# Performance work log

Measured on AMD Instinct MI355X. Metric: run time of the kernel, lower is better.

Reference implementation:

```python
import jax, jax.numpy as jnp
import numpy as np

NUM_GRAPHS = 512
EPS = 1e-5

def squash(x):
    # capsule squash: (|x|^2 / (1 + |x|^2)) * x / |x|
    n2 = jnp.sum(x * x, axis=-1, keepdims=True)
    return (n2 / (1.0 + n2)) * x * jax.lax.rsqrt(n2 + 1e-12)

def setup_inputs():
    key = jax.random.key(0)
    ks = jax.random.split(key, 16)
    N, E, F, H, L, C = 100000, 600000, 128, 128, 3, 2
    x = jax.random.normal(ks[0], (N, F), jnp.float32)
    edge_index = jax.random.randint(ks[1], (2, E), 0, N)
    batch = jnp.sort(jax.random.randint(ks[2], (N,), 0, NUM_GRAPHS))
    def lin(k, i, o):
        return (jax.random.normal(k, (i, o), jnp.float32) / np.sqrt(i)).astype(jnp.float32)
    return {
        'x': x, 'edge_index': edge_index, 'batch': batch,
        'bn_gamma': jnp.ones((F,), jnp.float32), 'bn_beta': jnp.zeros((F,), jnp.float32),
        'W0': lin(ks[3], F, H), 'b0': jnp.zeros((H,), jnp.float32),
        'W1': lin(ks[4], H, H), 'b1': jnp.zeros((H,), jnp.float32),
        'W2': lin(ks[5], H, H), 'b2': jnp.zeros((H,), jnp.float32),
        'tar_w': (jax.random.normal(ks[6], (L, H), jnp.float32) / np.sqrt(H)).astype(jnp.float32),
        'lin1_w': lin(ks[7], 3 * H, H), 'lin1_b': jnp.zeros((H,), jnp.float32),
        'lin2_w': lin(ks[8], H, C), 'lin2_b': jnp.zeros((C,), jnp.float32),
    }

def reference(x, edge_index, batch, bn_gamma, bn_beta, W0, b0, W1, b1, W2, b2,
              tar_w, lin1_w, lin1_b, lin2_w, lin2_b):
    N, G = x.shape[0], NUM_GRAPHS
    # input BatchNorm1d (training-mode batch statistics)
    mu = jnp.mean(x, 0)
    var = jnp.var(x, 0)
    h = (x - mu) * jax.lax.rsqrt(var + EPS) * bn_gamma + bn_beta
    # remove_self_loops + add_remaining_self_loops ~= append diagonal with weight 1
    loops = jnp.arange(N)
    src = jnp.concatenate([edge_index[0], loops])
    dst = jnp.concatenate([edge_index[1], loops])
    w = jnp.ones((src.shape[0],), h.dtype)
    # GCN symmetric normalization D^-1/2 A D^-1/2
    deg = jax.ops.segment_sum(w, dst, num_segments=N)
    dinv = jax.lax.rsqrt(jnp.maximum(deg, 1e-12))
    norm = dinv[src] * w * dinv[dst]  # [E+N]
    ones_n = jnp.ones((N,), h.dtype)
    cnt = jax.ops.segment_sum(ones_n, batch, num_segments=G)  # nodes per graph
    cnt_safe = jnp.maximum(cnt, 1.0)[:, None]
    graph_rep = jnp.zeros((G, 3 * W0.shape[1]), h.dtype)
    loss_stability = jnp.zeros((), h.dtype)
    for i, (W, b) in enumerate([(W0, b0), (W1, b1), (W2, b2)]):
        m = h @ W  # [N, H]
        agg = jax.ops.segment_sum(norm[:, None] * m[src], dst, num_segments=N) + b
        h = squash(agg)
        loss_stability = loss_stability + jnp.mean((agg - h) ** 2)
        # Task-Aware Readout: node attention then fused sum / mean / max scatters
        attn = h @ tar_w[i]  # [N]
        x_wsum = jax.ops.segment_sum(attn[:, None] * h, batch, num_segments=G)
        x_mean = jax.ops.segment_sum(h, batch, num_segments=G) / cnt_safe
        x_max = jax.ops.segment_max(h, batch, num_segments=G)
        x_max = jnp.where(cnt[:, None] > 0, x_max, 0.0)
        graph_rep = graph_rep + jnp.concatenate([x_wsum, x_mean, x_max], axis=-1)
    z = jax.nn.relu(graph_rep @ lin1_w + lin1_b)
    z = z @ lin2_w + lin2_b
    return jax.nn.log_softmax(z, axis=-1)
```

## Files before the change

kernel.cpp:

```cpp
#include <hip/hip_runtime.h>
#include <hip/hip_bf16.h>
#include <math.h>

#define BN_EPS 1e-5f
#define BN_BLOCKS 512
#define NCHUNK 256

typedef __attribute__((ext_vector_type(8)))  short short8v;
typedef __attribute__((ext_vector_type(16))) float f32x16;

__device__ __forceinline__ unsigned short f2bf(float f){
  union { float f; unsigned u; } v; v.f = f;
  unsigned r = v.u + 0x7FFFu + ((v.u >> 16) & 1u);
  return (unsigned short)(r >> 16);
}
__device__ __forceinline__ float bf2f(unsigned short b){
  union { unsigned u; float f; } v; v.u = ((unsigned)b) << 16;
  return v.f;
}
__device__ __forceinline__ float2 bfpair(unsigned u){
  union { unsigned u; float f; } lo, hi;
  lo.u = u << 16;
  hi.u = u & 0xFFFF0000u;
  return make_float2(lo.f, hi.f);
}
__device__ __forceinline__ unsigned packbf(float a, float b){
  return (unsigned)f2bf(a) | ((unsigned)f2bf(b) << 16);
}

__global__ __launch_bounds__(256) void bn_part(const float* __restrict__ x,
                                               float* __restrict__ part, int total4){
  const float4* x4 = (const float4*)x;
  int stride = gridDim.x * blockDim.x;
  float4 s = make_float4(0.f,0.f,0.f,0.f);
  float4 q = make_float4(0.f,0.f,0.f,0.f);
  for (int idx = blockIdx.x*blockDim.x + threadIdx.x; idx < total4; idx += stride){
    float4 v = x4[idx];
    s.x += v.x; s.y += v.y; s.z += v.z; s.w += v.w;
    q.x += v.x*v.x; q.y += v.y*v.y; q.z += v.z*v.z; q.w += v.w*v.w;
  }
  __shared__ float4 shs[256], shq[256];
  shs[threadIdx.x] = s; shq[threadIdx.x] = q;
  __syncthreads();
  if (threadIdx.x < 32){
    int c4 = threadIdx.x;
    float4 ts = shs[c4], tq = shq[c4];
    #pragma unroll
    for (int j = 1; j < 8; ++j){
      float4 os = shs[c4 + j*32], oq = shq[c4 + j*32];
      ts.x += os.x; ts.y += os.y; ts.z += os.z; ts.w += os.w;
      tq.x += oq.x; tq.y += oq.y; tq.z += oq.z; tq.w += oq.w;
    }
    float* pb = part + (size_t)blockIdx.x * 256;
    *(float4*)(pb + c4*4)       = ts;
    *(float4*)(pb + 128 + c4*4) = tq;
  }
}

__global__ __launch_bounds__(256) void bn_reduce(const float* __restrict__ part,
                                                 const float* __restrict__ gamma,
                                                 const float* __restrict__ beta,
                                                 float* __restrict__ scale,
                                                 float* __restrict__ shift, int N){
  int t = threadIdx.x;
  float a0=0.f,a1=0.f,a2=0.f,a3=0.f,a4=0.f,a5=0.f,a6=0.f,a7=0.f;
  for (int b = 0; b < BN_BLOCKS; b += 8){
    a0 += part[(size_t)(b+0)*256 + t];
    a1 += part[(size_t)(b+1)*256 + t];
    a2 += part[(size_t)(b+2)*256 + t];
    a3 += part[(size_t)(b+3)*256 + t];
    a4 += part[(size_t)(b+4)*256 + t];
    a5 += part[(size_t)(b+5)*256 + t];
    a6 += part[(size_t)(b+6)*256 + t];
    a7 += part[(size_t)(b+7)*256 + t];
  }
  float acc = ((a0+a1)+(a2+a3)) + ((a4+a5)+(a6+a7));
  __shared__ float sh[256];
  sh[t] = acc;
  __syncthreads();
  if (t < 128){
    float mu  = sh[t] / (float)N;
    float var = sh[t+128] / (float)N - mu*mu;
    float sc  = gamma[t] * rsqrtf(var + BN_EPS);
    scale[t] = sc;
    shift[t] = beta[t] - mu*sc;
  }
}


__global__ __launch_bounds__(256) void chunk_hist(const int* __restrict__ dst,
                                                  int* __restrict__ hist2,
                                                  int E, int NB, int CH){
  __shared__ int lh[512];
  for (int i = threadIdx.x; i < NB; i += 256) lh[i] = 0;
  __syncthreads();
  int c = blockIdx.x;
  int e0 = c*CH, e1 = min(e0 + CH, E);
  for (int e = e0 + threadIdx.x; e < e1; e += 256)
    atomicAdd(&lh[dst[e] >> 8], 1);
  __syncthreads();
  for (int i = threadIdx.x; i < NB; i += 256)
    hist2[c*NB + i] = lh[i];
}

__global__ __launch_bounds__(512) void chunk_scan(const int* __restrict__ hist2,
                                                  int* __restrict__ offs2,
                                                  int* __restrict__ bbase,
                                                  int NB, int E){
  __shared__ int tot[512];
  int b = threadIdx.x;
  int total = 0;
  if (b < NB){
    for (int c = 0; c < NCHUNK; c += 8){
      int h0 = hist2[(c+0)*NB + b], h1 = hist2[(c+1)*NB + b];
      int h2 = hist2[(c+2)*NB + b], h3 = hist2[(c+3)*NB + b];
      int h4 = hist2[(c+4)*NB + b], h5 = hist2[(c+5)*NB + b];
      int h6 = hist2[(c+6)*NB + b], h7 = hist2[(c+7)*NB + b];
      total += ((h0+h1)+(h2+h3)) + ((h4+h5)+(h6+h7));
    }
  }
  tot[b] = (b < NB) ? total : 0;
  __syncthreads();
  int v = tot[b];
  for (int d = 1; d < 512; d <<= 1){
    int u = (b >= d) ? tot[b-d] : 0;
    __syncthreads();
    tot[b] += u;
    __syncthreads();
  }
  if (b < NB){
    int base = tot[b] - v;
    bbase[b] = base;
    int run = base;
    for (int c = 0; c < NCHUNK; c += 8){
      int h0 = hist2[(c+0)*NB + b], h1 = hist2[(c+1)*NB + b];
      int h2 = hist2[(c+2)*NB + b], h3 = hist2[(c+3)*NB + b];
      int h4 = hist2[(c+4)*NB + b], h5 = hist2[(c+5)*NB + b];
      int h6 = hist2[(c+6)*NB + b], h7 = hist2[(c+7)*NB + b];
      offs2[(c+0)*NB + b] = run; run += h0;
      offs2[(c+1)*NB + b] = run; run += h1;
      offs2[(c+2)*NB + b] = run; run += h2;
      offs2[(c+3)*NB + b] = run; run += h3;
      offs2[(c+4)*NB + b] = run; run += h4;
      offs2[(c+5)*NB + b] = run; run += h5;
      offs2[(c+6)*NB + b] = run; run += h6;
      offs2[(c+7)*NB + b] = run; run += h7;
    }
  }
  if (b == 0) bbase[NB] = E;
}

__global__ __launch_bounds__(256) void chunk_scatter(const int* __restrict__ src,
                                                     const int* __restrict__ dst,
                                                     const int* __restrict__ offs2,
                                                     unsigned* __restrict__ ebuf,
                                                     int E, int NB, int CH){
  __shared__ int lcur[512];
  int c = blockIdx.x;
  for (int i = threadIdx.x; i < NB; i += 256) lcur[i] = offs2[c*NB + i];
  __syncthreads();
  int e0 = c*CH, e1 = min(e0 + CH, E);
  for (int e = e0 + threadIdx.x; e < e1; e += 256){
    int d = dst[e];
    int b = d >> 8;
    int pos = atomicAdd(&lcur[b], 1);
    ebuf[pos] = ((unsigned)(d & 255) << 24) | (unsigned)src[e];
  }
}

__global__ __launch_bounds__(256) void bucket_sort(const unsigned* __restrict__ ebuf,
                                                   const int* __restrict__ bbase,
                                                   int* __restrict__ csrs,
                                                   int* __restrict__ rowstart,
                                                   float* __restrict__ dinv,
                                                   int N, int E, int NB){
  int b = blockIdx.x;
  int base = bbase[b];
  int end  = bbase[b+1];
  int len  = end - base;
  int tid = threadIdx.x;
  __shared__ int cnt[256];
  __shared__ int pref[256];
  cnt[tid] = 0;
  __syncthreads();
  for (int i = tid; i < len; i += 256)
    atomicAdd(&cnt[ebuf[base + i] >> 24], 1);
  __syncthreads();
  int v = cnt[tid];
  pref[tid] = v;
  __syncthreads();
  for (int d = 1; d < 256; d <<= 1){
    int u = (tid >= d) ? pref[tid-d] : 0;
    __syncthreads();
    pref[tid] += u;
    __syncthreads();
  }
  int excl = pref[tid] - v;
  int node = b*256 + tid;
  if (node < N){
    rowstart[node] = base + excl;
    dinv[node] = rsqrtf((float)v + 1.0f);
  }
  cnt[tid] = excl;
  __syncthreads();
  for (int i = tid; i < len; i += 256){
    unsigned r = ebuf[base + i];
    int pos = atomicAdd(&cnt[r >> 24], 1);
    csrs[base + pos] = (int)(r & 0xFFFFFFu);
  }
  if (b == NB-1 && tid == 0) rowstart[N] = E;
}

__global__ void gbounds(const int* __restrict__ batch, int* __restrict__ gstart, int N, int G){
  int g = blockIdx.x*blockDim.x + threadIdx.x;
  if (g > G) return;
  int lo = 0, hi = N;
  while (lo < hi){ int mid = (lo+hi)>>1; if (batch[mid] < g) lo = mid+1; else hi = mid; }
  gstart[g] = lo;
}

__global__ void prep_w(const float* __restrict__ W0, const float* __restrict__ W1,
                       const float* __restrict__ W2, const float* __restrict__ scale,
                       unsigned short* __restrict__ Wh){
  int idx = blockIdx.x*blockDim.x + threadIdx.x;
  if (idx >= 3*16384) return;
  int l = idx >> 14, r = idx & 16383, c = r >> 7, k = r & 127;
  const float* W = (l==0) ? W0 : (l==1) ? W1 : W2;
  float v = W[k*128 + c];
  if (l == 0) v *= scale[k];
  Wh[idx] = f2bf(v);
}

__global__ __launch_bounds__(128) void prep_bias0(const float* __restrict__ b0,
                                                  const float* __restrict__ shift,
                                                  const float* __restrict__ W0,
                                                  float* __restrict__ bias0p){
  int j = threadIdx.x;
  __shared__ float sh[128];
  sh[j] = shift[j];
  __syncthreads();
  float s = b0[j];
  for (int c = 0; c < 128; ++c) s += sh[c] * W0[c*128 + j];
  bias0p[j] = s;
}

template<int CVT>
__global__ __launch_bounds__(512) void gemm_mfma(
    const float* __restrict__ A32, const unsigned short* __restrict__ A16,
    const unsigned short* __restrict__ Bh, unsigned short* __restrict__ C, int N){
  __shared__ unsigned short Ah[64*128];
  int tid = threadIdx.x;
  int r0 = blockIdx.x * 64;
  int w = tid >> 6, lane = tid & 63;
  int rt = w & 1;
  int ct = (w >> 1) * 32;
  int lrow = 32*rt + (lane & 31);
  int khalf = lane >> 5;
  int c0 = ct + (lane & 31);
  const unsigned short* bh0 = Bh + (size_t)c0*128 + khalf*8;

  short8v bhf[8];
  #pragma unroll
  for (int s = 0; s < 8; ++s) bhf[s] = *(const short8v*)(bh0 + s*16);

  if (CVT){
    #pragma unroll
    for (int it = 0; it < 4; ++it){
      int idx = tid + it*512;
      int row = idx >> 5;
      int c4  = idx & 31;
      int r = r0 + row;
      float4 av = (r < N) ? *(const float4*)(A32 + (size_t)r*128 + c4*4)
                          : make_float4(0.f,0.f,0.f,0.f);
      int byte0 = (c4*8) ^ ((row & 15) << 4);
      uint2 p = make_uint2(packbf(av.x, av.y), packbf(av.z, av.w));
      *(uint2*)((char*)Ah + row*256 + byte0) = p;
    }
  } else {
    #pragma unroll
    for (int it = 0; it < 2; ++it){
      int idx = tid + it*512;
      int row = idx >> 4;
      int c8  = idx & 15;
      int r = r0 + row;
      uint4 v = (r < N) ? *(const uint4*)(A16 + (size_t)r*128 + c8*8)
                        : make_uint4(0,0,0,0);
      int byte0 = (c8*16) ^ ((row & 15) << 4);
      *(uint4*)((char*)Ah + row*256 + byte0) = v;
    }
  }
  __syncthreads();

  f32x16 acc = {};
  const char* AhB = (const char*)Ah + lrow*256;
  int sw = (lrow & 15) << 4;
  #pragma unroll
  for (int s = 0; s < 8; ++s){
    int abyte = (s*32 + khalf*16) ^ sw;
    short8v a = *(const short8v*)(AhB + abyte);
    acc = __builtin_amdgcn_mfma_f32_32x32x16_bf16(a, bhf[s], acc, 0, 0, 0);
  }

  #pragma unroll
  for (int r = 0; r < 16; ++r){
    int row = r0 + 32*rt + (r & 3) + 8*(r >> 2) + 4*khalf;
    if (row < N) C[(size_t)row*128 + c0] = f2bf(acc[r]);
  }
}

__global__ __launch_bounds__(256) void gather_squash(
    const unsigned short* __restrict__ m, const int* __restrict__ rowstart,
    const int* __restrict__ csrs, const float* __restrict__ dinv,
    const float* __restrict__ bias, const float* __restrict__ tar,
    unsigned short* __restrict__ h, float* __restrict__ attn, int N){
  int node = blockIdx.x*8 + (threadIdx.x >> 5);
  if (node >= N) return;
  int lane = threadIdx.x & 31;
  const uint2* m2 = (const uint2*)m;
  float dv = dinv[node];
  float sn = dv*dv;
  uint2 sv = m2[(size_t)node*32 + lane];
  float2 p0 = bfpair(sv.x), p1 = bfpair(sv.y);
  float a0 = p0.x*sn, a1 = p0.y*sn, a2 = p1.x*sn, a3 = p1.y*sn;
  int j0 = rowstart[node], j1 = rowstart[node+1];

  for (int base = j0; base < j1; base += 32){
    int cnt = j1 - base; if (cnt > 32) cnt = 32;
    int sidx = 0; float swt = 0.f;
    if (lane < cnt){
      sidx = csrs[base + lane];
      swt  = dinv[sidx] * dv;
    }
    int t = 0;
    for (; t + 4 <= cnt; t += 4){
      int s0 = __shfl(sidx, t, 32),   s1 = __shfl(sidx, t+1, 32);
      int s2 = __shfl(sidx, t+2, 32), s3 = __shfl(sidx, t+3, 32);
      float w0 = __shfl(swt, t, 32),   w1 = __shfl(swt, t+1, 32);
      float w2 = __shfl(swt, t+2, 32), w3 = __shfl(swt, t+3, 32);
      uint2 u0 = m2[(size_t)s0*32 + lane];
      uint2 u1 = m2[(size_t)s1*32 + lane];
      uint2 u2 = m2[(size_t)s2*32 + lane];
      uint2 u3 = m2[(size_t)s3*32 + lane];
      float2 q0, q1;
      q0 = bfpair(u0.x); q1 = bfpair(u0.y);
      a0 += w0*q0.x; a1 += w0*q0.y; a2 += w0*q1.x; a3 += w0*q1.y;
      q0 = bfpair(u1.x); q1 = bfpair(u1.y);
      a0 += w1*q0.x; a1 += w1*q0.y; a2 += w1*q1.x; a3 += w1*q1.y;
      q0 = bfpair(u2.x); q1 = bfpair(u2.y);
      a0 += w2*q0.x; a1 += w2*q0.y; a2 += w2*q1.x; a3 += w2*q1.y;
      q0 = bfpair(u3.x); q1 = bfpair(u3.y);
      a0 += w3*q0.x; a1 += w3*q0.y; a2 += w3*q1.x; a3 += w3*q1.y;
    }
    if (cnt - t >= 2){
      int s0 = __shfl(sidx, t, 32), s1 = __shfl(sidx, t+1, 32);
      float w0 = __shfl(swt, t, 32), w1 = __shfl(swt, t+1, 32);
      uint2 u0 = m2[(size_t)s0*32 + lane];
      uint2 u1 = m2[(size_t)s1*32 + lane];
      float2 q0 = bfpair(u0.x), q1 = bfpair(u0.y);
      a0 += w0*q0.x; a1 += w0*q0.y; a2 += w0*q1.x; a3 += w0*q1.y;
      q0 = bfpair(u1.x); q1 = bfpair(u1.y);
      a0 += w1*q0.x; a1 += w1*q0.y; a2 += w1*q1.x; a3 += w1*q1.y;
      t += 2;
    }
    if (t < cnt){
      int s0 = __shfl(sidx, t, 32);
      float w0 = __shfl(swt, t, 32);
      uint2 u0 = m2[(size_t)s0*32 + lane];
      float2 q0 = bfpair(u0.x), q1 = bfpair(u0.y);
      a0 += w0*q0.x; a1 += w0*q0.y; a2 += w0*q1.x; a3 += w0*q1.y;
    }
  }

  float4 bv = ((const float4*)bias)[lane];
  a0 += bv.x; a1 += bv.y; a2 += bv.z; a3 += bv.w;
  float n2 = a0*a0 + a1*a1 + a2*a2 + a3*a3;
  #pragma unroll
  for (int o = 16; o > 0; o >>= 1) n2 += __shfl_xor(n2, o);
  float sc = (n2/(1.f+n2)) * rsqrtf(n2 + 1e-12f);
  float h0 = a0*sc, h1 = a1*sc, h2 = a2*sc, h3 = a3*sc;
  ((uint2*)(h + (size_t)node*128))[lane] = make_uint2(packbf(h0,h1), packbf(h2,h3));
  float4 tv = ((const float4*)tar)[lane];
  float at = h0*tv.x + h1*tv.y + h2*tv.z + h3*tv.w;
  #pragma unroll
  for (int o = 16; o > 0; o >>= 1) at += __shfl_xor(at, o);
  if (lane == 0) attn[node] = at;
}

__global__ __launch_bounds__(1024) void readout(const unsigned short* __restrict__ h,
                                                const float* __restrict__ attn,
                                                const int* __restrict__ gstart,
                                                float* __restrict__ grep){
  int g = blockIdx.x;
  int t   = threadIdx.x & 63;
  int grp = threadIdx.x >> 6;
  int a = gstart[g], b = gstart[g+1];
  float wsx = 0.f, wsy = 0.f, smx_ = 0.f, smy_ = 0.f;
  float mxx = -INFINITY, mxy = -INFINITY;
  for (int n = a + grp; n < b; n += 16){
    unsigned u = ((const unsigned*)(h + (size_t)n*128))[t];
    float2 v = bfpair(u);
    float at = attn[n];
    wsx += at*v.x; wsy += at*v.y;
    smx_ += v.x;  smy_ += v.y;
    mxx = fmaxf(mxx, v.x); mxy = fmaxf(mxy, v.y);
  }
  __shared__ float2 sws[16][64], ssm[16][64], smx[16][64];
  sws[grp][t] = make_float2(wsx, wsy);
  ssm[grp][t] = make_float2(smx_, smy_);
  smx[grp][t] = make_float2(mxx, mxy);
  __syncthreads();
  if (grp == 0){
    #pragma unroll
    for (int j = 1; j < 16; ++j){
      float2 ow = sws[j][t], os = ssm[j][t], om = smx[j][t];
      wsx += ow.x; wsy += ow.y;
      smx_ += os.x; smy_ += os.y;
      mxx = fmaxf(mxx, om.x); mxy = fmaxf(mxy, om.y);
    }
    int cnt = b - a;
    float inv = 1.f / fmaxf((float)cnt, 1.f);
    if (cnt == 0){ mxx = 0.f; mxy = 0.f; }
    grep[(size_t)g*384 + t*2]           += wsx;
    grep[(size_t)g*384 + t*2 + 1]       += wsy;
    grep[(size_t)g*384 + 128 + t*2]     += smx_*inv;
    grep[(size_t)g*384 + 128 + t*2 + 1] += smy_*inv;
    grep[(size_t)g*384 + 256 + t*2]     += mxx;
    grep[(size_t)g*384 + 256 + t*2 + 1] += mxy;
  }
}

__global__ __launch_bounds__(128) void classify(const float* __restrict__ grep,
                                                const float* __restrict__ w1, const float* __restrict__ b1,
                                                const float* __restrict__ w2, const float* __restrict__ b2,
                                                float* __restrict__ out){
  int g = blockIdx.x, t = threadIdx.x;
  __shared__ float gr[384];
  for (int i = t; i < 384; i += 128) gr[i] = grep[(size_t)g*384 + i];
  __syncthreads();
  float z = b1[t];
  for (int k = 0; k < 384; ++k) z += gr[k]*w1[k*128 + t];
  z = fmaxf(z, 0.f);
  float c0 = z*w2[t*2 + 0], c1 = z*w2[t*2 + 1];
  #pragma unroll
  for (int o = 32; o > 0; o >>= 1){ c0 += __shfl_xor(c0, o); c1 += __shfl_xor(c1, o); }
  __shared__ float r0s[2], r1s[2];
  if ((t & 63) == 0){ r0s[t>>6] = c0; r1s[t>>6] = c1; }
  __syncthreads();
  if (t == 0){
    float z0 = r0s[0] + r0s[1] + b2[0];
    float z1 = r1s[0] + r1s[1] + b2[1];
    float mm = fmaxf(z0, z1);
    float lse = mm + logf(expf(z0-mm) + expf(z1-mm));
    out[g*2 + 0] = z0 - lse;
    out[g*2 + 1] = z1 - lse;
  }
}

extern "C" void kernel_launch(void* const* d_in, const int* in_sizes, int n_in,
                              void* d_out, int out_size, void* d_ws, size_t ws_size,
                              hipStream_t stream) {
  const float* x     = (const float*)d_in[0];
  const int*   ei    = (const int*)d_in[1];
  const int*   batch = (const int*)d_in[2];
  const float* gamma = (const float*)d_in[3];
  const float* beta  = (const float*)d_in[4];
  const float* W0    = (const float*)d_in[5];
  const float* b0    = (const float*)d_in[6];
  const float* W1    = (const float*)d_in[7];
  const float* b1    = (const float*)d_in[8];
  const float* W2    = (const float*)d_in[9];
  const float* b2    = (const float*)d_in[10];
  const float* tar   = (const float*)d_in[11];
  const float* l1w   = (const float*)d_in[12];
  const float* l1b   = (const float*)d_in[13];
  const float* l2w   = (const float*)d_in[14];
  const float* l2b   = (const float*)d_in[15];
  float* out = (float*)d_out;

  int N = in_sizes[0] / 128;
  int E = in_sizes[1] / 2;
  int G = out_size / 2;
  const int* srcp = ei;
  const int* dstp = ei + E;

  char* wsb = (char*)d_ws;
  size_t off = 0;
  auto alloc = [&](size_t bytes)->char*{
    char* p = wsb + off; off += (bytes + 255) & ~(size_t)255; return p;
  };
  unsigned short* h = (unsigned short*)alloc((size_t)N*128*2);
  unsigned short* m = (unsigned short*)alloc((size_t)N*128*2);
  float* attn    = (float*)alloc((size_t)N*4);
  float* dinv    = (float*)alloc((size_t)N*4);
  int*   rowst   = (int*)  alloc((size_t)(N+1)*4);
  int*   csrs    = (int*)  alloc((size_t)E*4);
  unsigned* ebuf = (unsigned*)alloc((size_t)E*4);
  int*   hist2   = (int*)  alloc((size_t)NCHUNK*512*4);
  int*   offs2   = (int*)  alloc((size_t)NCHUNK*512*4);
  int*   bbase   = (int*)  alloc(513*4);
  int*   gstart  = (int*)  alloc((size_t)(G+1)*4);
  float* grep    = (float*)alloc((size_t)G*384*4);
  float* stats   = (float*)alloc(2*128*4);
  float* bias0p  = (float*)alloc(128*4);
  float* part    = (float*)alloc((size_t)BN_BLOCKS*256*4);
  unsigned short* Wh = (unsigned short*)alloc(3*16384*2);
  (void)ws_size;

  float* scale  = stats;
  float* shift  = stats + 128;

  int NB = (N + 255) >> 8;
  int CH = (E + NCHUNK - 1) / NCHUNK;
  hipMemsetAsync(grep, 0, (size_t)G*384*4, stream);

  chunk_hist<<<NCHUNK, 256, 0, stream>>>(dstp, hist2, E, NB, CH);
  chunk_scan<<<1, 512, 0, stream>>>(hist2, offs2, bbase, NB, E);
  chunk_scatter<<<NCHUNK, 256, 0, stream>>>(srcp, dstp, offs2, ebuf, E, NB, CH);
  bucket_sort<<<NB, 256, 0, stream>>>(ebuf, bbase, csrs, rowst, dinv, N, E, NB);
  gbounds<<<(G+1+255)/256, 256, 0, stream>>>(batch, gstart, N, G);

  bn_part<<<BN_BLOCKS, 256, 0, stream>>>(x, part, N*32);
  bn_reduce<<<1, 256, 0, stream>>>(part, gamma, beta, scale, shift, N);
  prep_w<<<(3*16384+255)/256, 256, 0, stream>>>(W0, W1, W2, scale, Wh);
  prep_bias0<<<1, 128, 0, stream>>>(b0, shift, W0, bias0p);

  const float* bs[3] = {bias0p, b1, b2};
  int nb64 = (N + 63) / 64;
  for (int l = 0; l < 3; ++l){
    if (l == 0)
      gemm_mfma<1><<<nb64, 512, 0, stream>>>(x, nullptr, Wh, m, N);
    else
      gemm_mfma<0><<<nb64, 512, 0, stream>>>(nullptr, h, Wh + l*16384, m, N);
    gather_squash<<<(N+7)/8, 256, 0, stream>>>(m, rowst, csrs, dinv, bs[l], tar + l*128, h, attn, N);
    readout<<<G, 1024, 0, stream>>>(h, attn, gstart, grep);
  }
  classify<<<G, 128, 0, stream>>>(grep, l1w, l1b, l2w, l2b, out);
}
```

Baseline: 277.5 us.

## Fuse readout into gather-squash with atomic pooling and merge setup kernels

The separate readout kernel is removed. Its work moves into the gather/squash kernel, which pools the weighted sum, plain sum and max per graph. It does this with shared-memory atomics for up to 8 graphs per block and falls back to global atomics otherwise, using an order-preserving float-to-uint map for max. The mean divide and the sum of the three per-layer maxes move into classify. The many small setup kernels (histogram+BN partials, scan+BN reduce+graph bounds, sort+weight prep+bias) are merged into fewer launches. This removes the attn buffer, the readback of h per layer, and several launch gaps, in exchange for atomic contention and non-deterministic float summation order.

Result: slower. 590.5 us (+112.8%).

```diff
diff --git a/kernel.cpp b/kernel.cpp
--- a/kernel.cpp
+++ b/kernel.cpp
@@ -3,7 +3,6 @@
 #include <math.h>
 
 #define BN_EPS 1e-5f
-#define BN_BLOCKS 512
 #define NCHUNK 256
 
 typedef __attribute__((ext_vector_type(8)))  short short8v;
@@ -13,10 +12,6 @@
   union { float f; unsigned u; } v; v.f = f;
   unsigned r = v.u + 0x7FFFu + ((v.u >> 16) & 1u);
   return (unsigned short)(r >> 16);
-}
-__device__ __forceinline__ float bf2f(unsigned short b){
-  union { unsigned u; float f; } v; v.u = ((unsigned)b) << 16;
-  return v.f;
 }
 __device__ __forceinline__ float2 bfpair(unsigned u){
   union { unsigned u; float f; } lo, hi;
@@ -27,127 +22,138 @@
 __device__ __forceinline__ unsigned packbf(float a, float b){
   return (unsigned)f2bf(a) | ((unsigned)f2bf(b) << 16);
 }
-
-__global__ __launch_bounds__(256) void bn_part(const float* __restrict__ x,
-                                               float* __restrict__ part, int total4){
-  const float4* x4 = (const float4*)x;
-  int stride = gridDim.x * blockDim.x;
-  float4 s = make_float4(0.f,0.f,0.f,0.f);
-  float4 q = make_float4(0.f,0.f,0.f,0.f);
-  for (int idx = blockIdx.x*blockDim.x + threadIdx.x; idx < total4; idx += stride){
-    float4 v = x4[idx];
-    s.x += v.x; s.y += v.y; s.z += v.z; s.w += v.w;
-    q.x += v.x*v.x; q.y += v.y*v.y; q.z += v.z*v.z; q.w += v.w*v.w;
-  }
-  __shared__ float4 shs[256], shq[256];
-  shs[threadIdx.x] = s; shq[threadIdx.x] = q;
-  __syncthreads();
-  if (threadIdx.x < 32){
-    int c4 = threadIdx.x;
-    float4 ts = shs[c4], tq = shq[c4];
-    #pragma unroll
-    for (int j = 1; j < 8; ++j){
-      float4 os = shs[c4 + j*32], oq = shq[c4 + j*32];
-      ts.x += os.x; ts.y += os.y; ts.z += os.z; ts.w += os.w;
-      tq.x += oq.x; tq.y += oq.y; tq.z += oq.z; tq.w += oq.w;
-    }
-    float* pb = part + (size_t)blockIdx.x * 256;
-    *(float4*)(pb + c4*4)       = ts;
-    *(float4*)(pb + 128 + c4*4) = tq;
-  }
-}
-
-__global__ __launch_bounds__(256) void bn_reduce(const float* __restrict__ part,
-                                                 const float* __restrict__ gamma,
-                                                 const float* __restrict__ beta,
-                                                 float* __restrict__ scale,
-                                                 float* __restrict__ shift, int N){
+__device__ __forceinline__ unsigned fmap(float f){
+  union { float f; unsigned u; } v; v.f = f;
+  return (v.u & 0x80000000u) ? ~v.u : (v.u | 0x80000000u);
+}
+__device__ __forceinline__ float funmap(unsigned u){
+  union { unsigned u; float f; } v;
+  v.u = (u & 0x80000000u) ? (u & 0x7FFFFFFFu) : ~u;
+  return v.f;
+}
+
+__global__ __launch_bounds__(256) void k_hist_bn(const int* __restrict__ dst,
+                                                 int* __restrict__ hist2, int E, int NB, int CH,
+                                                 const float* __restrict__ x,
+                                                 float* __restrict__ part, int total4){
+  int tid = threadIdx.x;
+  if (blockIdx.x < NCHUNK){
+    __shared__ int lh[512];
+    for (int i = tid; i < NB; i += 256) lh[i] = 0;
+    __syncthreads();
+    int c = blockIdx.x;
+    int e0 = c*CH, e1 = min(e0 + CH, E);
+    for (int e = e0 + tid; e < e1; e += 256)
+      atomicAdd(&lh[dst[e] >> 8], 1);
+    __syncthreads();
+    for (int i = tid; i < NB; i += 256)
+      hist2[c*NB + i] = lh[i];
+  } else {
+    const float4* x4 = (const float4*)x;
+    int bb = blockIdx.x - NCHUNK;
+    int stride = 512 * 256;
+    float4 s = make_float4(0.f,0.f,0.f,0.f);
+    float4 q = make_float4(0.f,0.f,0.f,0.f);
+    for (int idx = bb*256 + tid; idx < total4; idx += stride){
+      float4 v = x4[idx];
+      s.x += v.x; s.y += v.y; s.z += v.z; s.w += v.w;
+      q.x += v.x*v.x; q.y += v.y*v.y; q.z += v.z*v.z; q.w += v.w*v.w;
+    }
+    __shared__ float4 shs[256], shq[256];
+    shs[tid] = s; shq[tid] = q;
+    __syncthreads();
+    if (tid < 32){
+      int c4 = tid;
+      float4 ts = shs[c4], tq = shq[c4];
+      #pragma unroll
+      for (int j = 1; j < 8; ++j){
+        float4 os = shs[c4 + j*32], oq = shq[c4 + j*32];
+        ts.x += os.x; ts.y += os.y; ts.z += os.z; ts.w += os.w;
+        tq.x += oq.x; tq.y += oq.y; tq.z += oq.z; tq.w += oq.w;
+      }
+      float* pb = part + (size_t)bb * 256;
+      *(float4*)(pb + c4*4)       = ts;
+      *(float4*)(pb + 128 + c4*4) = tq;
+    }
+  }
+}
+
+__global__ __launch_bounds__(512) void k_scan_red_gb(const int* __restrict__ hist2,
+                                                     int* __restrict__ offs2,
+                                                     int* __restrict__ bbase, int NB, int E,
+                                                     const float* __restrict__ part,
+                                                     const float* __restrict__ gamma,
+                                                     const float* __restrict__ beta,
+                                                     float* __restrict__ scale,
+                                                     float* __restrict__ shift, int N,
+                                                     const int* __restrict__ batch,
+                                                     int* __restrict__ gstart, int G){
   int t = threadIdx.x;
-  float a0=0.f,a1=0.f,a2=0.f,a3=0.f,a4=0.f,a5=0.f,a6=0.f,a7=0.f;
-  for (int b = 0; b < BN_BLOCKS; b += 8){
-    a0 += part[(size_t)(b+0)*256 + t];
-    a1 += part[(size_t)(b+1)*256 + t];
-    a2 += part[(size_t)(b+2)*256 + t];
-    a3 += part[(size_t)(b+3)*256 + t];
-    a4 += part[(size_t)(b+4)*256 + t];
-    a5 += part[(size_t)(b+5)*256 + t];
-    a6 += part[(size_t)(b+6)*256 + t];
-    a7 += part[(size_t)(b+7)*256 + t];
-  }
-  float acc = ((a0+a1)+(a2+a3)) + ((a4+a5)+(a6+a7));
-  __shared__ float sh[256];
-  sh[t] = acc;
-  __syncthreads();
-  if (t < 128){
-    float mu  = sh[t] / (float)N;
-    float var = sh[t+128] / (float)N - mu*mu;
-    float sc  = gamma[t] * rsqrtf(var + BN_EPS);
-    scale[t] = sc;
-    shift[t] = beta[t] - mu*sc;
-  }
-}
-
-
-__global__ __launch_bounds__(256) void chunk_hist(const int* __restrict__ dst,
-                                                  int* __restrict__ hist2,
-                                                  int E, int NB, int CH){
-  __shared__ int lh[512];
-  for (int i = threadIdx.x; i < NB; i += 256) lh[i] = 0;
-  __syncthreads();
-  int c = blockIdx.x;
-  int e0 = c*CH, e1 = min(e0 + CH, E);
-  for (int e = e0 + threadIdx.x; e < e1; e += 256)
-    atomicAdd(&lh[dst[e] >> 8], 1);
-  __syncthreads();
-  for (int i = threadIdx.x; i < NB; i += 256)
-    hist2[c*NB + i] = lh[i];
-}
-
-__global__ __launch_bounds__(512) void chunk_scan(const int* __restrict__ hist2,
-                                                  int* __restrict__ offs2,
-                                                  int* __restrict__ bbase,
-                                                  int NB, int E){
-  __shared__ int tot[512];
-  int b = threadIdx.x;
-  int total = 0;
-  if (b < NB){
-    for (int c = 0; c < NCHUNK; c += 8){
-      int h0 = hist2[(c+0)*NB + b], h1 = hist2[(c+1)*NB + b];
-      int h2 = hist2[(c+2)*NB + b], h3 = hist2[(c+3)*NB + b];
-      int h4 = hist2[(c+4)*NB + b], h5 = hist2[(c+5)*NB + b];
-      int h6 = hist2[(c+6)*NB + b], h7 = hist2[(c+7)*NB + b];
-      total += ((h0+h1)+(h2+h3)) + ((h4+h5)+(h6+h7));
-    }
-  }
-  tot[b] = (b < NB) ? total : 0;
-  __syncthreads();
-  int v = tot[b];
-  for (int d = 1; d < 512; d <<= 1){
-    int u = (b >= d) ? tot[b-d] : 0;
-    __syncthreads();
-    tot[b] += u;
-    __syncthreads();
-  }
-  if (b < NB){
-    int base = tot[b] - v;
-    bbase[b] = base;
-    int run = base;
-    for (int c = 0; c < NCHUNK; c += 8){
-      int h0 = hist2[(c+0)*NB + b], h1 = hist2[(c+1)*NB + b];
-      int h2 = hist2[(c+2)*NB + b], h3 = hist2[(c+3)*NB + b];
-      int h4 = hist2[(c+4)*NB + b], h5 = hist2[(c+5)*NB + b];
-      int h6 = hist2[(c+6)*NB + b], h7 = hist2[(c+7)*NB + b];
-      offs2[(c+0)*NB + b] = run; run += h0;
-      offs2[(c+1)*NB + b] = run; run += h1;
-      offs2[(c+2)*NB + b] = run; run += h2;
-      offs2[(c+3)*NB + b] = run; run += h3;
-      offs2[(c+4)*NB + b] = run; run += h4;
-      offs2[(c+5)*NB + b] = run; run += h5;
-      offs2[(c+6)*NB + b] = run; run += h6;
-      offs2[(c+7)*NB + b] = run; run += h7;
-    }
-  }
-  if (b == 0) bbase[NB] = E;
+  if (blockIdx.x == 0){
+    __shared__ int tot[512];
+    int b = t;
+    int total = 0;
+    if (b < NB){
+      for (int c = 0; c < NCHUNK; c += 8){
+        int h0 = hist2[(c+0)*NB + b], h1 = hist2[(c+1)*NB + b];
+        int h2 = hist2[(c+2)*NB + b], h3 = hist2[(c+3)*NB + b];
+        int h4 = hist2[(c+4)*NB + b], h5 = hist2[(c+5)*NB + b];
+        int h6 = hist2[(c+6)*NB + b], h7 = hist2[(c+7)*NB + b];
+        total += ((h0+h1)+(h2+h3)) + ((h4+h5)+(h6+h7));
+      }
+    }
+    tot[b] = (b < NB) ? total : 0;
+    __syncthreads();
+    int v = tot[b];
+    for (int d = 1; d < 512; d <<= 1){
+      int u = (b >= d) ? tot[b-d] : 0;
+      __syncthreads();
+      tot[b] += u;
+      __syncthreads();
+    }
+    if (b < NB){
+      int base = tot[b] - v;
+      bbase[b] = base;
+      int run = base;
+      for (int c = 0; c < NCHUNK; ++c){
+        offs2[c*NB + b] = run;
+        run += hist2[c*NB + b];
+      }
+    }
+    if (b == 0) bbase[NB] = E;
+  } else if (blockIdx.x == 1){
+    if (t < 256){
+      float a0=0.f,a1=0.f,a2=0.f,a3=0.f,a4=0.f,a5=0.f,a6=0.f,a7=0.f;
+      for (int b = 0; b < 512; b += 8){
+        a0 += part[(size_t)(b+0)*256 + t];
+        a1 += part[(size_t)(b+1)*256 + t];
+        a2 += part[(size_t)(b+2)*256 + t];
+        a3 += part[(size_t)(b+3)*256 + t];
+        a4 += part[(size_t)(b+4)*256 + t];
+        a5 += part[(size_t)(b+5)*256 + t];
+        a6 += part[(size_t)(b+6)*256 + t];
+        a7 += part[(size_t)(b+7)*256 + t];
+      }
+      float acc = ((a0+a1)+(a2+a3)) + ((a4+a5)+(a6+a7));
+      __shared__ float sh[256];
+      sh[t] = acc;
+      __syncthreads();
+      if (t < 128){
+        float mu  = sh[t] / (float)N;
+        float var = sh[t+128] / (float)N - mu*mu;
+        float sc  = gamma[t] * rsqrtf(var + BN_EPS);
+        scale[t] = sc;
+        shift[t] = beta[t] - mu*sc;
+      }
+    }
+  } else {
+    int g = (blockIdx.x - 2)*512 + t;
+    if (g <= G){
+      int lo = 0, hi = N;
+      while (lo < hi){ int mid = (lo+hi)>>1; if (batch[mid] < g) lo = mid+1; else hi = mid; }
+      gstart[g] = lo;
+    }
+  }
 }
 
 __global__ __launch_bounds__(256) void chunk_scatter(const int* __restrict__ src,
@@ -168,80 +174,73 @@
   }
 }
 
-__global__ __launch_bounds__(256) void bucket_sort(const unsigned* __restrict__ ebuf,
+__global__ __launch_bounds__(256) void k_sort_prep(const unsigned* __restrict__ ebuf,
                                                    const int* __restrict__ bbase,
                                                    int* __restrict__ csrs,
                                                    int* __restrict__ rowstart,
                                                    float* __restrict__ dinv,
-                                                   int N, int E, int NB){
-  int b = blockIdx.x;
-  int base = bbase[b];
-  int end  = bbase[b+1];
-  int len  = end - base;
+                                                   int N, int E, int NB,
+                                                   const float* __restrict__ W0,
+                                                   const float* __restrict__ W1,
+                                                   const float* __restrict__ W2,
+                                                   const float* __restrict__ scale,
+                                                   unsigned short* __restrict__ Wh,
+                                                   const float* __restrict__ b0,
+                                                   const float* __restrict__ shift,
+                                                   float* __restrict__ bias0p){
   int tid = threadIdx.x;
-  __shared__ int cnt[256];
-  __shared__ int pref[256];
-  cnt[tid] = 0;
-  __syncthreads();
-  for (int i = tid; i < len; i += 256)
-    atomicAdd(&cnt[ebuf[base + i] >> 24], 1);
-  __syncthreads();
-  int v = cnt[tid];
-  pref[tid] = v;
-  __syncthreads();
-  for (int d = 1; d < 256; d <<= 1){
-    int u = (tid >= d) ? pref[tid-d] : 0;
-    __syncthreads();
-    pref[tid] += u;
-    __syncthreads();
-  }
-  int excl = pref[tid] - v;
-  int node = b*256 + tid;
-  if (node < N){
-    rowstart[node] = base + excl;
-    dinv[node] = rsqrtf((float)v + 1.0f);
-  }
-  cnt[tid] = excl;
-  __syncthreads();
-  for (int i = tid; i < len; i += 256){
-    unsigned r = ebuf[base + i];
-    int pos = atomicAdd(&cnt[r >> 24], 1);
-    csrs[base + pos] = (int)(r & 0xFFFFFFu);
-  }
-  if (b == NB-1 && tid == 0) rowstart[N] = E;
-}
-
-__global__ void gbounds(const int* __restrict__ batch, int* __restrict__ gstart, int N, int G){
-  int g = blockIdx.x*blockDim.x + threadIdx.x;
-  if (g > G) return;
-  int lo = 0, hi = N;
-  while (lo < hi){ int mid = (lo+hi)>>1; if (batch[mid] < g) lo = mid+1; else hi = mid; }
-  gstart[g] = lo;
-}
-
-__global__ void prep_w(const float* __restrict__ W0, const float* __restrict__ W1,
-                       const float* __restrict__ W2, const float* __restrict__ scale,
-                       unsigned short* __restrict__ Wh){
-  int idx = blockIdx.x*blockDim.x + threadIdx.x;
-  if (idx >= 3*16384) return;
-  int l = idx >> 14, r = idx & 16383, c = r >> 7, k = r & 127;
-  const float* W = (l==0) ? W0 : (l==1) ? W1 : W2;
-  float v = W[k*128 + c];
-  if (l == 0) v *= scale[k];
-  Wh[idx] = f2bf(v);
-}
-
-__global__ __launch_bounds__(128) void prep_bias0(const float* __restrict__ b0,
-                                                  const float* __restrict__ shift,
-                                                  const float* __restrict__ W0,
-                                                  float* __restrict__ bias0p){
-  int j = threadIdx.x;
-  __shared__ float sh[128];
-  sh[j] = shift[j];
-  __syncthreads();
-  float s = b0[j];
-  for (int c = 0; c < 128; ++c) s += sh[c] * W0[c*128 + j];
-  bias0p[j] = s;
+  if ((int)blockIdx.x < NB){
+    int b = blockIdx.x;
+    int base = bbase[b];
+    int end  = bbase[b+1];
+    int len  = end - base;
+    __shared__ int cnt[256];
+    __shared__ int pref[256];
+    cnt[tid] = 0;
+    __syncthreads();
+    for (int i = tid; i < len; i += 256)
+      atomicAdd(&cnt[ebuf[base + i] >> 24], 1);
+    __syncthreads();
+    int v = cnt[tid];
+    pref[tid] = v;
+    __syncthreads();
+    for (int d = 1; d < 256; d <<= 1){
+      int u = (tid >= d) ? pref[tid-d] : 0;
+      __syncthreads();
+      pref[tid] += u;
+      __syncthreads();
+    }
+    int excl = pref[tid] - v;
+    int node = b*256 + tid;
+    if (node < N){
+      rowstart[node] = base + excl;
+      dinv[node] = rsqrtf((float)v + 1.0f);
+    }
+    cnt[tid] = excl;
+    __syncthreads();
+    for (int i = tid; i < len; i += 256){
+      unsigned r = ebuf[base + i];
+      int pos = atomicAdd(&cnt[r >> 24], 1);
+      csrs[base + pos] = (int)(r & 0xFFFFFFu);
+    }
+    if (b == NB-1 && tid == 0) rowstart[N] = E;
+  } else if ((int)blockIdx.x < NB + 192){
+    int idx = (blockIdx.x - NB)*256 + tid;
+    int l = idx >> 14, r = idx & 16383, c = r >> 7, k = r & 127;
+    const float* W = (l==0) ? W0 : (l==1) ? W1 : W2;
+    float v = W[k*128 + c];
+    if (l == 0) v *= scale[k];
+    Wh[idx] = f2bf(v);
+  } else {
+    __shared__ float sh[128];
+    if (tid < 128) sh[tid] = shift[tid];
+    __syncthreads();
+    if (tid < 128){
+      float s = b0[tid];
+      for (int c = 0; c < 128; ++c) s += sh[c] * W0[c*128 + tid];
+      bias0p[tid] = s;
+    }
+  }
 }
 
 template<int CVT>
@@ -308,134 +307,167 @@
   }
 }
 
-__global__ __launch_bounds__(256) void gather_squash(
+template<int LAST>
+__global__ __launch_bounds__(256) void gather_ro(
     const unsigned short* __restrict__ m, const int* __restrict__ rowstart,
     const int* __restrict__ csrs, const float* __restrict__ dinv,
     const float* __restrict__ bias, const float* __restrict__ tar,
-    unsigned short* __restrict__ h, float* __restrict__ attn, int N){
-  int node = blockIdx.x*8 + (threadIdx.x >> 5);
-  if (node >= N) return;
-  int lane = threadIdx.x & 31;
-  const uint2* m2 = (const uint2*)m;
-  float dv = dinv[node];
-  float sn = dv*dv;
-  uint2 sv = m2[(size_t)node*32 + lane];
-  float2 p0 = bfpair(sv.x), p1 = bfpair(sv.y);
-  float a0 = p0.x*sn, a1 = p0.y*sn, a2 = p1.x*sn, a3 = p1.y*sn;
-  int j0 = rowstart[node], j1 = rowstart[node+1];
-
-  for (int base = j0; base < j1; base += 32){
-    int cnt = j1 - base; if (cnt > 32) cnt = 32;
-    int sidx = 0; float swt = 0.f;
-    if (lane < cnt){
-      sidx = csrs[base + lane];
-      swt  = dinv[sidx] * dv;
-    }
-    int t = 0;
-    for (; t + 4 <= cnt; t += 4){
-      int s0 = __shfl(sidx, t, 32),   s1 = __shfl(sidx, t+1, 32);
-      int s2 = __shfl(sidx, t+2, 32), s3 = __shfl(sidx, t+3, 32);
-      float w0 = __shfl(swt, t, 32),   w1 = __shfl(swt, t+1, 32);
-      float w2 = __shfl(swt, t+2, 32), w3 = __shfl(swt, t+3, 32);
-      uint2 u0 = m2[(size_t)s0*32 + lane];
-      uint2 u1 = m2[(size_t)s1*32 + lane];
-      uint2 u2 = m2[(size_t)s2*32 + lane];
-      uint2 u3 = m2[(size_t)s3*32 + lane];
-      float2 q0, q1;
-      q0 = bfpair(u0.x); q1 = bfpair(u0.y);
-      a0 += w0*q0.x; a1 += w0*q0.y; a2 += w0*q1.x; a3 += w0*q1.y;
-      q0 = bfpair(u1.x); q1 = bfpair(u1.y);
-      a0 += w1*q0.x; a1 += w1*q0.y; a2 += w1*q1.x; a3 += w1*q1.y;
-      q0 = bfpair(u2.x); q1 = bfpair(u2.y);
-      a0 += w2*q0.x; a1 += w2*q0.y; a2 += w2*q1.x; a3 += w2*q1.y;
-      q0 = bfpair(u3.x); q1 = bfpair(u3.y);
-      a0 += w3*q0.x; a1 += w3*q0.y; a2 += w3*q1.x; a3 += w3*q1.y;
-    }
-    if (cnt - t >= 2){
-      int s0 = __shfl(sidx, t, 32), s1 = __shfl(sidx, t+1, 32);
-      float w0 = __shfl(swt, t, 32), w1 = __shfl(swt, t+1, 32);
-      uint2 u0 = m2[(size_t)s0*32 + lane];
-      uint2 u1 = m2[(size_t)s1*32 + lane];
-      float2 q0 = bfpair(u0.x), q1 = bfpair(u0.y);
-      a0 += w0*q0.x; a1 += w0*q0.y; a2 += w0*q1.x; a3 += w0*q1.y;
-      q0 = bfpair(u1.x); q1 = bfpair(u1.y);
-      a0 += w1*q0.x; a1 += w1*q0.y; a2 += w1*q1.x; a3 += w1*q1.y;
-      t += 2;
-    }
-    if (t < cnt){
-      int s0 = __shfl(sidx, t, 32);
-      float w0 = __shfl(swt, t, 32);
-      uint2 u0 = m2[(size_t)s0*32 + lane];
-      float2 q0 = bfpair(u0.x), q1 = bfpair(u0.y);
-      a0 += w0*q0.x; a1 += w0*q0.y; a2 += w0*q1.x; a3 += w0*q1.y;
-    }
-  }
-
-  float4 bv = ((const float4*)bias)[lane];
-  a0 += bv.x; a1 += bv.y; a2 += bv.z; a3 += bv.w;
-  float n2 = a0*a0 + a1*a1 + a2*a2 + a3*a3;
-  #pragma unroll
-  for (int o = 16; o > 0; o >>= 1) n2 += __shfl_xor(n2, o);
-  float sc = (n2/(1.f+n2)) * rsqrtf(n2 + 1e-12f);
-  float h0 = a0*sc, h1 = a1*sc, h2 = a2*sc, h3 = a3*sc;
-  ((uint2*)(h + (size_t)node*128))[lane] = make_uint2(packbf(h0,h1), packbf(h2,h3));
-  float4 tv = ((const float4*)tar)[lane];
-  float at = h0*tv.x + h1*tv.y + h2*tv.z + h3*tv.w;
-  #pragma unroll
-  for (int o = 16; o > 0; o >>= 1) at += __shfl_xor(at, o);
-  if (lane == 0) attn[node] = at;
-}
-
-__global__ __launch_bounds__(1024) void readout(const unsigned short* __restrict__ h,
-                                                const float* __restrict__ attn,
+    const int* __restrict__ batch, unsigned short* __restrict__ h,
+    float* __restrict__ grepF, unsigned* __restrict__ grepM, int N, int G){
+  __shared__ float lws[8][128];
+  __shared__ float lsm[8][128];
+  __shared__ unsigned lmx[8][128];
+  __shared__ int smax;
+  int tid = threadIdx.x;
+  for (int i = tid; i < 8*128; i += 256){
+    ((float*)lws)[i] = 0.f; ((float*)lsm)[i] = 0.f; ((unsigned*)lmx)[i] = 0u;
+  }
+  if (tid == 0) smax = 0;
+  __syncthreads();
+
+  int node = blockIdx.x*8 + (tid >> 5);
+  int lane = tid & 31;
+  int nf = blockIdx.x*8; if (nf >= N) nf = N-1;
+  int g0 = batch[nf];
+  bool active = (node < N);
+  float h0=0.f,h1=0.f,h2=0.f,h3=0.f,at=0.f;
+  int g = g0, slot = 0;
+
+  if (active){
+    const uint2* m2 = (const uint2*)m;
+    float dv = dinv[node];
+    float sn = dv*dv;
+    uint2 sv = m2[(size_t)node*32 + lane];
+    float2 p0 = bfpair(sv.x), p1 = bfpair(sv.y);
+    float a0 = p0.x*sn, a1 = p0.y*sn, a2 = p1.x*sn, a3 = p1.y*sn;
+    int j0 = rowstart[node], j1 = rowstart[node+1];
+
+    for (int base = j0; base < j1; base += 32){
+      int cnt = j1 - base; if (cnt > 32) cnt = 32;
+      int sidx = 0; float swt = 0.f;
+      if (lane < cnt){
+        sidx = csrs[base + lane];
+        swt  = dinv[sidx] * dv;
+      }
+      int t = 0;
+      for (; t + 4 <= cnt; t += 4){
+        int s0 = __shfl(sidx, t, 32),   s1 = __shfl(sidx, t+1, 32);
+        int s2 = __shfl(sidx, t+2, 32), s3 = __shfl(sidx, t+3, 32);
+        float w0 = __shfl(swt, t, 32),   w1 = __shfl(swt, t+1, 32);
+        float w2 = __shfl(swt, t+2, 32), w3 = __shfl(swt, t+3, 32);
+        uint2 u0 = m2[(size_t)s0*32 + lane];
+        uint2 u1 = m2[(size_t)s1*32 + lane];
+        uint2 u2 = m2[(size_t)s2*32 + lane];
+        uint2 u3 = m2[(size_t)s3*32 + lane];
+        float2 q0, q1;
+        q0 = bfpair(u0.x); q1 = bfpair(u0.y);
+        a0 += w0*q0.x; a1 += w0*q0.y; a2 += w0*q1.x; a3 += w0*q1.y;
+        q0 = bfpair(u1.x); q1 = bfpair(u1.y);
+        a0 += w1*q0.x; a1 += w1*q0.y; a2 += w1*q1.x; a3 += w1*q1.y;
+        q0 = bfpair(u2.x); q1 = bfpair(u2.y);
+        a0 += w2*q0.x; a1 += w2*q0.y; a2 += w2*q1.x; a3 += w2*q1.y;
+        q0 = bfpair(u3.x); q1 = bfpair(u3.y);
+        a0 += w3*q0.x; a1 += w3*q0.y; a2 += w3*q1.x; a3 += w3*q1.y;
+      }
+      if (cnt - t >= 2){
+        int s0 = __shfl(sidx, t, 32), s1 = __shfl(sidx, t+1, 32);
+        float w0 = __shfl(swt, t, 32), w1 = __shfl(swt, t+1, 32);
+        uint2 u0 = m2[(size_t)s0*32 + lane];
+        uint2 u1 = m2[(size_t)s1*32 + lane];
+        float2 q0 = bfpair(u0.x), q1 = bfpair(u0.y);
+        a0 += w0*q0.x; a1 += w0*q0.y; a2 += w0*q1.x; a3 += w0*q1.y;
+        q0 = bfpair(u1.x); q1 = bfpair(u1.y);
+        a0 += w1*q0.x; a1 += w1*q0.y; a2 += w1*q1.x; a3 += w1*q1.y;
+        t += 2;
+      }
+      if (t < cnt){
+        int s0 = __shfl(sidx, t, 32);
+        float w0 = __shfl(swt, t, 32);
+        uint2 u0 = m2[(size_t)s0*32 + lane];
+        float2 q0 = bfpair(u0.x), q1 = bfpair(u0.y);
+        a0 += w0*q0.x; a1 += w0*q0.y; a2 += w0*q1.x; a3 += w0*q1.y;
+      }
+    }
+
+    float4 bv = ((const float4*)bias)[lane];
+    a0 += bv.x; a1 += bv.y; a2 += bv.z; a3 += bv.w;
+    float n2 = a0*a0 + a1*a1 + a2*a2 + a3*a3;
+    #pragma unroll
+    for (int o = 16; o > 0; o >>= 1) n2 += __shfl_xor(n2, o);
+    float sc = (n2/(1.f+n2)) * rsqrtf(n2 + 1e-12f);
+    h0 = a0*sc; h1 = a1*sc; h2 = a2*sc; h3 = a3*sc;
+    if (!LAST)
+      ((uint2*)(h + (size_t)node*128))[lane] = make_uint2(packbf(h0,h1), packbf(h2,h3));
+    float4 tv = ((const float4*)tar)[lane];
+    at = h0*tv.x + h1*tv.y + h2*tv.z + h3*tv.w;
+    #pragma unroll
+    for (int o = 16; o > 0; o >>= 1) at += __shfl_xor(at, o);
+    g = batch[node];
+    slot = g - g0;
+  }
+
+  if (active){
+    if (slot < 8){
+      int f = lane*4;
+      atomicAdd(&lws[slot][f+0], at*h0); atomicAdd(&lws[slot][f+1], at*h1);
+      atomicAdd(&lws[slot][f+2], at*h2); atomicAdd(&lws[slot][f+3], at*h3);
+      atomicAdd(&lsm[slot][f+0], h0);    atomicAdd(&lsm[slot][f+1], h1);
+      atomicAdd(&lsm[slot][f+2], h2);    atomicAdd(&lsm[slot][f+3], h3);
+      atomicMax(&lmx[slot][f+0], fmap(h0)); atomicMax(&lmx[slot][f+1], fmap(h1));
+      atomicMax(&lmx[slot][f+2], fmap(h2)); atomicMax(&lmx[slot][f+3], fmap(h3));
+      if (lane == 0) atomicMax(&smax, slot);
+    } else {
+      int f = lane*4;
+      atomicAdd(&grepF[(size_t)g*128 + f+0], at*h0);
+      atomicAdd(&grepF[(size_t)g*128 + f+1], at*h1);
+      atomicAdd(&grepF[(size_t)g*128 + f+2], at*h2);
+      atomicAdd(&grepF[(size_t)g*128 + f+3], at*h3);
+      atomicAdd(&grepF[((size_t)G + g)*128 + f+0], h0);
+      atomicAdd(&grepF[((size_t)G + g)*128 + f+1], h1);
+      atomicAdd(&grepF[((size_t)G + g)*128 + f+2], h2);
+      atomicAdd(&grepF[((size_t)G + g)*128 + f+3], h3);
+      atomicMax(&grepM[(size_t)g*128 + f+0], fmap(h0));
+      atomicMax(&grepM[(size_t)g*128 + f+1], fmap(h1));
+      atomicMax(&grepM[(size_t)g*128 + f+2], fmap(h2));
+      atomicMax(&grepM[(size_t)g*128 + f+3], fmap(h3));
+    }
+  }
+  __syncthreads();
+  int ms = smax;
+  if (tid < 128){
+    for (int s = 0; s <= ms; ++s){
+      int gg = g0 + s;
+      if (gg < G){
+        float vw = lws[s][tid], vs = lsm[s][tid];
+        unsigned vm = lmx[s][tid];
+        atomicAdd(&grepF[(size_t)gg*128 + tid], vw);
+        atomicAdd(&grepF[((size_t)G + gg)*128 + tid], vs);
+        if (vm) atomicMax(&grepM[(size_t)gg*128 + tid], vm);
+      }
+    }
+  }
+}
+
+__global__ __launch_bounds__(128) void classify(const float* __restrict__ grepF,
+                                                const unsigned* __restrict__ grepM,
                                                 const int* __restrict__ gstart,
-                                                float* __restrict__ grep){
-  int g = blockIdx.x;
-  int t   = threadIdx.x & 63;
-  int grp = threadIdx.x >> 6;
-  int a = gstart[g], b = gstart[g+1];
-  float wsx = 0.f, wsy = 0.f, smx_ = 0.f, smy_ = 0.f;
-  float mxx = -INFINITY, mxy = -INFINITY;
-  for (int n = a + grp; n < b; n += 16){
-    unsigned u = ((const unsigned*)(h + (size_t)n*128))[t];
-    float2 v = bfpair(u);
-    float at = attn[n];
-    wsx += at*v.x; wsy += at*v.y;
-    smx_ += v.x;  smy_ += v.y;
-    mxx = fmaxf(mxx, v.x); mxy = fmaxf(mxy, v.y);
-  }
-  __shared__ float2 sws[16][64], ssm[16][64], smx[16][64];
-  sws[grp][t] = make_float2(wsx, wsy);
-  ssm[grp][t] = make_float2(smx_, smy_);
-  smx[grp][t] = make_float2(mxx, mxy);
-  __syncthreads();
-  if (grp == 0){
-    #pragma unroll
-    for (int j = 1; j < 16; ++j){
-      float2 ow = sws[j][t], os = ssm[j][t], om = smx[j][t];
-      wsx += ow.x; wsy += ow.y;
-      smx_ += os.x; smy_ += os.y;
-      mxx = fmaxf(mxx, om.x); mxy = fmaxf(mxy, om.y);
-    }
-    int cnt = b - a;
-    float inv = 1.f / fmaxf((float)cnt, 1.f);
-    if (cnt == 0){ mxx = 0.f; mxy = 0.f; }
-    grep[(size_t)g*384 + t*2]           += wsx;
-    grep[(size_t)g*384 + t*2 + 1]       += wsy;
-    grep[(size_t)g*384 + 128 + t*2]     += smx_*inv;
-    grep[(size_t)g*384 + 128 + t*2 + 1] += smy_*inv;
-    grep[(size_t)g*384 + 256 + t*2]     += mxx;
-    grep[(size_t)g*384 + 256 + t*2 + 1] += mxy;
-  }
-}
-
-__global__ __launch_bounds__(128) void classify(const float* __restrict__ grep,
                                                 const float* __restrict__ w1, const float* __restrict__ b1,
                                                 const float* __restrict__ w2, const float* __restrict__ b2,
-                                                float* __restrict__ out){
+                                                float* __restrict__ out, int G){
   int g = blockIdx.x, t = threadIdx.x;
   __shared__ float gr[384];
-  for (int i = t; i < 384; i += 128) gr[i] = grep[(size_t)g*384 + i];
+  int a = gstart[g], b = gstart[g+1];
+  int cnt = b - a;
+  float inv = 1.f / fmaxf((float)cnt, 1.f);
+  gr[t]       = grepF[(size_t)g*128 + t];
+  gr[128 + t] = grepF[((size_t)G + g)*128 + t] * inv;
+  float mx = 0.f;
+  if (cnt > 0){
+    #pragma unroll
+    for (int l = 0; l < 3; ++l)
+      mx += funmap(grepM[((size_t)l*G + g)*128 + t]);
+  }
+  gr[256 + t] = mx;
   __syncthreads();
   float z = b1[t];
   for (int k = 0; k < 384; ++k) z += gr[k]*w1[k*128 + t];
@@ -490,7 +522,6 @@
   };
   unsigned short* h = (unsigned short*)alloc((size_t)N*128*2);
   unsigned short* m = (unsigned short*)alloc((size_t)N*128*2);
-  float* attn    = (float*)alloc((size_t)N*4);
   float* dinv    = (float*)alloc((size_t)N*4);
   int*   rowst   = (int*)  alloc((size_t)(N+1)*4);
   int*   csrs    = (int*)  alloc((size_t)E*4);
@@ -499,10 +530,11 @@
   int*   offs2   = (int*)  alloc((size_t)NCHUNK*512*4);
   int*   bbase   = (int*)  alloc(513*4);
   int*   gstart  = (int*)  alloc((size_t)(G+1)*4);
-  float* grep    = (float*)alloc((size_t)G*384*4);
+  float* grepF   = (float*)alloc((size_t)(2*G)*128*4 + (size_t)(3*G)*128*4);
+  unsigned* grepM = (unsigned*)(grepF + (size_t)(2*G)*128);
   float* stats   = (float*)alloc(2*128*4);
   float* bias0p  = (float*)alloc(128*4);
-  float* part    = (float*)alloc((size_t)BN_BLOCKS*256*4);
+  float* part    = (float*)alloc((size_t)512*256*4);
   unsigned short* Wh = (unsigned short*)alloc(3*16384*2);
   (void)ws_size;
 
@@ -511,18 +543,15 @@
 
   int NB = (N + 255) >> 8;
   int CH = (E + NCHUNK - 1) / NCHUNK;
-  hipMemsetAsync(grep, 0, (size_t)G*384*4, stream);
-
-  chunk_hist<<<NCHUNK, 256, 0, stream>>>(dstp, hist2, E, NB, CH);
-  chunk_scan<<<1, 512, 0, stream>>>(hist2, offs2, bbase, NB, E);
+  hipMemsetAsync(grepF, 0, (size_t)(5*G)*128*4, stream);
+
+  k_hist_bn<<<NCHUNK + 512, 256, 0, stream>>>(dstp, hist2, E, NB, CH, x, part, N*32);
+  k_scan_red_gb<<<4, 512, 0, stream>>>(hist2, offs2, bbase, NB, E,
+                                       part, gamma, beta, scale, shift, N,
+                                       batch, gstart, G);
   chunk_scatter<<<NCHUNK, 256, 0, stream>>>(srcp, dstp, offs2, ebuf, E, NB, CH);
-  bucket_sort<<<NB, 256, 0, stream>>>(ebuf, bbase, csrs, rowst, dinv, N, E, NB);
-  gbounds<<<(G+1+255)/256, 256, 0, stream>>>(batch, gstart, N, G);
-
-  bn_part<<<BN_BLOCKS, 256, 0, stream>>>(x, part, N*32);
-  bn_reduce<<<1, 256, 0, stream>>>(part, gamma, beta, scale, shift, N);
-  prep_w<<<(3*16384+255)/256, 256, 0, stream>>>(W0, W1, W2, scale, Wh);
-  prep_bias0<<<1, 128, 0, stream>>>(b0, shift, W0, bias0p);
+  k_sort_prep<<<NB + 193, 256, 0, stream>>>(ebuf, bbase, csrs, rowst, dinv, N, E, NB,
+                                            W0, W1, W2, scale, Wh, b0, shift, bias0p);
 
   const float* bs[3] = {bias0p, b1, b2};
   int nb64 = (N + 63) / 64;
@@ -531,8 +560,12 @@
       gemm_mfma<1><<<nb64, 512, 0, stream>>>(x, nullptr, Wh, m, N);
     else
       gemm_mfma<0><<<nb64, 512, 0, stream>>>(nullptr, h, Wh + l*16384, m, N);
-    gather_squash<<<(N+7)/8, 256, 0, stream>>>(m, rowst, csrs, dinv, bs[l], tar + l*128, h, attn, N);
-    readout<<<G, 1024, 0, stream>>>(h, attn, gstart, grep);
-  }
-  classify<<<G, 128, 0, stream>>>(grep, l1w, l1b, l2w, l2b, out);
-}
+    if (l < 2)
+      gather_ro<0><<<(N+7)/8, 256, 0, stream>>>(m, rowst, csrs, dinv, bs[l], tar + l*128,
+                                                batch, h, grepF, grepM + (size_t)l*G*128, N, G);
+    else
+      gather_ro<1><<<(N+7)/8, 256, 0, stream>>>(m, rowst, csrs, dinv, bs[l], tar + l*128,
+                                                batch, h, grepF, grepM + (size_t)l*G*128, N, G);
+  }
+  classify<<<G, 128, 0, stream>>>(grepF, grepM, gstart, l1w, l1b, l2w, l2b, out, G);
+}
```
